# Kernel tuning notes

Hardware: AMD Instinct MI355X
Metric: run time of the kernel (lower is better)

## Reference

```python
import jax, jax.numpy as jnp
import numpy as np

D = 512

def setup_inputs() -> dict:
    key = jax.random.key(0)
    ks = jax.random.split(key, 12)
    B, d, H, W = 128, D, 14, 14
    s = 1.0 / np.sqrt(d)
    s2 = 1.0 / np.sqrt(2 * d)
    return {
        "m_prev": jax.random.normal(ks[0], (B, d), dtype=jnp.float32),
        "KB": jax.random.normal(ks[1], (B, d, H, W), dtype=jnp.float32),
        "c_i": jax.random.normal(ks[2], (B, d), dtype=jnp.float32),
        # Linear params stored as [in, out] so y = x @ W + b
        "W_m": jax.random.uniform(ks[3], (d, d), jnp.float32, -s, s),
        "b_m": jax.random.uniform(ks[4], (d,), jnp.float32, -s, s),
        "W_kb": jax.random.uniform(ks[5], (d, d), jnp.float32, -s, s),
        "b_kb": jax.random.uniform(ks[6], (d,), jnp.float32, -s, s),
        "W_merge": jax.random.uniform(ks[7], (2 * d, d), jnp.float32, -s2, s2),
        "b_merge": jax.random.uniform(ks[8], (d,), jnp.float32, -s2, s2),
        "W_attn": jax.random.uniform(ks[9], (d, 1), jnp.float32, -s, s),
        "b_attn": jax.random.uniform(ks[10], (1,), jnp.float32, -s, s),
    }


def reference(m_prev, KB, c_i, W_m, b_m, W_kb, b_kb, W_merge, b_merge, W_attn, b_attn):
    # m_prev: [B, d], KB: [B, d, H, W], c_i: [B, d]
    B, d, H, W = KB.shape
    KB_hw = jnp.transpose(KB, (0, 2, 3, 1))            # [B, H, W, d]
    _m_prev = (m_prev @ W_m + b_m)[:, None, None, :]   # [B, 1, 1, d]
    _KB = KB_hw @ W_kb + b_kb                          # [B, H, W, d]
    I = _m_prev * _KB                                  # [B, H, W, d]
    # merge: [I; KB] @ W_merge split into two halves to avoid the concat
    _I = I @ W_merge[:d] + KB_hw @ W_merge[d:] + b_merge  # [B, H, W, d]
    I2 = c_i[:, None, None, :] * _I                    # [B, H, W, d]
    mv = I2 @ W_attn + b_attn                          # [B, H, W, 1]
    # weighted spatial sum: sum over H*W of mv * KB_hw -> [B, d]
    m_new = jnp.einsum("bhwo,bhwd->bd", mv, KB_hw)
    return m_new
```

## Files before the change

### kernel.cpp

```cpp
#include <hip/hip_runtime.h>

#define D   512
#define HW  196
#define NS  8
#define MS  16


__global__ void k_stage1(const float* __restrict__ m_prev, const float* __restrict__ W_m,
                         const float* __restrict__ b_m, const float* __restrict__ c,
                         const float* __restrict__ W_attn, const float* __restrict__ W_merge,
                         float* __restrict__ p_part, float* __restrict__ t12_part) {
    const int bx = blockIdx.x;
    const int t  = threadIdx.x;
    __shared__ float xs[16][64];

    if (bx < 128) {
        const int jt = bx & 1, bt = (bx >> 1) & 7, kt = bx >> 4;
        const int j  = jt * 256 + t;
        const int b0 = bt * 16;
        const int k0 = kt * 64;
        for (int i = t; i < 16 * 64; i += 256)
            xs[i >> 6][i & 63] = m_prev[(b0 + (i >> 6)) * D + k0 + (i & 63)];
        __syncthreads();
        float acc[16];
        #pragma unroll
        for (int bb = 0; bb < 16; ++bb) acc[bb] = 0.f;
        for (int kk = 0; kk < 64; ++kk) {
            float wv = W_m[(k0 + kk) * D + j];
            #pragma unroll
            for (int bb = 0; bb < 16; ++bb) acc[bb] += xs[bb][kk] * wv;
        }
        const float bias = (kt == 0) ? b_m[j] : 0.f;
        #pragma unroll
        for (int bb = 0; bb < 16; ++bb)
            p_part[((size_t)kt * 128 + b0 + bb) * D + j] = acc[bb] + bias;
    } else {
        const int i2 = bx - 128;
        const int kkt = i2 & 3, bt = (i2 >> 2) & 7, jt = i2 >> 5;
        const int kk = kkt * 256 + t;
        const int b0 = bt * 16;
        const int j0 = jt * 64;
        for (int i = t; i < 16 * 64; i += 256) {
            int bb = i >> 6, jj = i & 63;
            xs[bb][jj] = c[(b0 + bb) * D + j0 + jj] * W_attn[j0 + jj];
        }
        __syncthreads();
        float acc[16];
        #pragma unroll
        for (int bb = 0; bb < 16; ++bb) acc[bb] = 0.f;
        const float4* wrow = (const float4*)&W_merge[(size_t)kk * D + j0];
        for (int q = 0; q < 16; ++q) {
            float4 w4 = wrow[q];
            #pragma unroll
            for (int bb = 0; bb < 16; ++bb)
                acc[bb] += xs[bb][4*q+0] * w4.x + xs[bb][4*q+1] * w4.y
                         + xs[bb][4*q+2] * w4.z + xs[bb][4*q+3] * w4.w;
        }
        #pragma unroll
        for (int bb = 0; bb < 16; ++bb)
            t12_part[((size_t)jt * 128 + b0 + bb) * 1024 + kk] = acc[bb];
    }
}

__global__ void k_stage2(const float* __restrict__ p_part, const float* __restrict__ t12_part,
                         const float* __restrict__ W_kb, const float* __restrict__ c,
                         const float* __restrict__ W_attn, const float* __restrict__ b_merge,
                         const float* __restrict__ b_kb, const float* __restrict__ b_attn,
                         float* __restrict__ w_part, float* __restrict__ beta) {
    const int bx = blockIdx.x;
    const int t  = threadIdx.x;
    __shared__ float rs[16][64];

    if (bx < 128) {
        const int kpt = bx & 1, bt = (bx >> 1) & 7, kt = bx >> 4;
        const int kp = kpt * 256 + t;
        const int b0 = bt * 16;
        const int k0 = kt * 64;
        for (int i = t; i < 16 * 64; i += 256) {
            int bb = i >> 6, kk = i & 63;
            int b = b0 + bb, k = k0 + kk;
            float pv = 0.f, tv = 0.f;
            #pragma unroll
            for (int s = 0; s < NS; ++s) {
                pv += p_part[((size_t)s * 128 + b) * D + k];
                tv += t12_part[((size_t)s * 128 + b) * 1024 + k];
            }
            rs[bb][kk] = pv * tv;
        }
        __syncthreads();
        float acc[16];
        #pragma unroll
        for (int bb = 0; bb < 16; ++bb) acc[bb] = 0.f;
        const float4* wrow = (const float4*)&W_kb[(size_t)kp * D + k0];
        for (int q = 0; q < 16; ++q) {
            float4 w4 = wrow[q];
            #pragma unroll
            for (int bb = 0; bb < 16; ++bb)
                acc[bb] += rs[bb][4*q+0] * w4.x + rs[bb][4*q+1] * w4.y
                         + rs[bb][4*q+2] * w4.z + rs[bb][4*q+3] * w4.w;
        }
        #pragma unroll
        for (int bb = 0; bb < 16; ++bb) {
            float extra = 0.f;
            if (kt == 0) {
                #pragma unroll
                for (int s = 0; s < NS; ++s)
                    extra += t12_part[((size_t)s * 128 + b0 + bb) * 1024 + 512 + kp];
            }
            w_part[((size_t)kt * 128 + b0 + bb) * D + kp] = acc[bb] + extra;
        }
    } else {
        const int b = bx - 128;
        float sum = 0.f;
        for (int j = t; j < D; j += 256) {
            float pv = 0.f, tv = 0.f;
            #pragma unroll
            for (int s = 0; s < NS; ++s) {
                pv += p_part[((size_t)s * 128 + b) * D + j];
                tv += t12_part[((size_t)s * 128 + b) * 1024 + j];
            }
            float u = c[b * D + j] * W_attn[j];
            sum += b_merge[j] * u + b_kb[j] * (pv * tv);
        }
        #pragma unroll
        for (int off = 32; off; off >>= 1) sum += __shfl_down(sum, off, 64);
        __shared__ float red[4];
        if ((t & 63) == 0) red[t >> 6] = sum;
        __syncthreads();
        if (t == 0) beta[b] = red[0] + red[1] + red[2] + red[3] + b_attn[0];
    }
}

__global__ void k_mv(const float* __restrict__ KB, const float* __restrict__ w_part,
                     float* __restrict__ mvp) {
    const int b  = blockIdx.x >> 4;
    const int ks = blockIdx.x & (MS - 1);
    const int t  = threadIdx.x;
    __shared__ float wl[32];
    if (t < 32) {
        float s = 0.f;
        #pragma unroll
        for (int q = 0; q < NS; ++q)
            s += w_part[((size_t)q * 128 + b) * D + ks * 32 + t];
        wl[t] = s;
    }
    __syncthreads();
    if (t < HW) {
        const float* kbp = KB + (size_t)b * D * HW + (size_t)ks * 32 * HW + t;
        float acc = 0.f;
        #pragma unroll
        for (int k = 0; k < 32; ++k) acc += kbp[(size_t)k * HW] * wl[k];
        mvp[((size_t)b * MS + ks) * HW + t] = acc;
    }
}

__global__ void k_mnew(const float* __restrict__ KB, const float* __restrict__ mvp,
                       const float* __restrict__ beta, float* __restrict__ out) {
    const int b  = blockIdx.x >> 4;
    const int kt = blockIdx.x & 15;
    const int t  = threadIdx.x;
    const int wave = t >> 6, lane = t & 63;
    __shared__ float4 mv4_s[49];

    if (t < HW) {
        float s = beta[b];
        #pragma unroll
        for (int q = 0; q < MS; ++q)
            s += mvp[((size_t)b * MS + q) * HW + t];
        ((float*)mv4_s)[t] = s;
    }
    __syncthreads();

    const float4 m4 = (lane < 49) ? mv4_s[lane] : make_float4(0.f, 0.f, 0.f, 0.f);
    #pragma unroll
    for (int i = 0; i < 8; ++i) {
        const int k = kt * 32 + wave * 8 + i;
        float p = 0.f;
        if (lane < 49) {
            float4 v = ((const float4*)(KB + ((size_t)b * D + k) * HW))[lane];
            p = v.x * m4.x + v.y * m4.y + v.z * m4.z + v.w * m4.w;
        }
        #pragma unroll
        for (int off = 32; off; off >>= 1) p += __shfl_xor(p, off, 64);
        if (lane == 0) out[(size_t)b * D + k] = p;
    }
}

extern "C" void kernel_launch(void* const* d_in, const int* in_sizes, int n_in,
                              void* d_out, int out_size, void* d_ws, size_t ws_size,
                              hipStream_t stream) {
    const float* m_prev  = (const float*)d_in[0];
    const float* KB      = (const float*)d_in[1];
    const float* c_i     = (const float*)d_in[2];
    const float* W_m     = (const float*)d_in[3];
    const float* b_m     = (const float*)d_in[4];
    const float* W_kb    = (const float*)d_in[5];
    const float* b_kb    = (const float*)d_in[6];
    const float* W_merge = (const float*)d_in[7];
    const float* b_merge = (const float*)d_in[8];
    const float* W_attn  = (const float*)d_in[9];
    const float* b_attn  = (const float*)d_in[10];
    float* out = (float*)d_out;

    float* ws       = (float*)d_ws;
    float* p_part   = ws;
    float* t12_part = ws + 524288;
    float* w_part   = ws + 1572864;
    float* beta     = ws + 2097152;
    float* mvp      = ws + 2097280;

    k_stage1<<<384, 256, 0, stream>>>(m_prev, W_m, b_m, c_i, W_attn, W_merge,
                                      p_part, t12_part);
    k_stage2<<<256, 256, 0, stream>>>(p_part, t12_part, W_kb, c_i, W_attn,
                                      b_merge, b_kb, b_attn, w_part, beta);
    k_mv  <<<2048, 256, 0, stream>>>(KB, w_part, mvp);
    k_mnew<<<2048, 256, 0, stream>>>(KB, mvp, beta, out);
}
```

Measured before the change: 51.13 us.

## Fuse stage2 W_kb projection and beta into the KB matvec kernel

```diff
diff --git a/kernel.cpp b/kernel.cpp
--- a/kernel.cpp
+++ b/kernel.cpp
@@ -62,92 +62,69 @@
     }
 }
 
-__global__ void k_stage2(const float* __restrict__ p_part, const float* __restrict__ t12_part,
-                         const float* __restrict__ W_kb, const float* __restrict__ c,
-                         const float* __restrict__ W_attn, const float* __restrict__ b_merge,
-                         const float* __restrict__ b_kb, const float* __restrict__ b_attn,
-                         float* __restrict__ w_part, float* __restrict__ beta) {
-    const int bx = blockIdx.x;
-    const int t  = threadIdx.x;
-    __shared__ float rs[16][64];
+__global__ __launch_bounds__(256, 4)
+void k_wmv(const float* __restrict__ KB, const float* __restrict__ p_part,
+           const float* __restrict__ t12_part, const float* __restrict__ W_kb,
+           const float* __restrict__ c, const float* __restrict__ W_attn,
+           const float* __restrict__ b_merge, const float* __restrict__ b_kb,
+           const float* __restrict__ b_attn, float* __restrict__ mvp) {
+    const int b    = blockIdx.x >> 4;
+    const int ks   = blockIdx.x & (MS - 1);
+    const int t    = threadIdx.x;
+    const int wave = t >> 6, lane = t & 63;
 
-    if (bx < 128) {
-        const int kpt = bx & 1, bt = (bx >> 1) & 7, kt = bx >> 4;
-        const int kp = kpt * 256 + t;
-        const int b0 = bt * 16;
-        const int k0 = kt * 64;
-        for (int i = t; i < 16 * 64; i += 256) {
-            int bb = i >> 6, kk = i & 63;
-            int b = b0 + bb, k = k0 + kk;
-            float pv = 0.f, tv = 0.f;
-            #pragma unroll
-            for (int s = 0; s < NS; ++s) {
-                pv += p_part[((size_t)s * 128 + b) * D + k];
-                tv += t12_part[((size_t)s * 128 + b) * 1024 + k];
-            }
-            rs[bb][kk] = pv * tv;
+    __shared__ float r_s[512];
+    __shared__ float wl[32];
+    __shared__ float winit[32];
+    __shared__ float redB[4];
+
+    for (int k = t; k < 512; k += 256) {
+        float pv = 0.f, tv = 0.f;
+        #pragma unroll
+        for (int s = 0; s < NS; ++s) {
+            pv += p_part[((size_t)s * 128 + b) * D + k];
+            tv += t12_part[((size_t)s * 128 + b) * 1024 + k];
         }
-        __syncthreads();
-        float acc[16];
+        r_s[k] = pv * tv;
+    }
+    if (t < 32) {
+        float s2 = 0.f;
         #pragma unroll
-        for (int bb = 0; bb < 16; ++bb) acc[bb] = 0.f;
-        const float4* wrow = (const float4*)&W_kb[(size_t)kp * D + k0];
-        for (int q = 0; q < 16; ++q) {
-            float4 w4 = wrow[q];
-            #pragma unroll
-            for (int bb = 0; bb < 16; ++bb)
-                acc[bb] += rs[bb][4*q+0] * w4.x + rs[bb][4*q+1] * w4.y
-                         + rs[bb][4*q+2] * w4.z + rs[bb][4*q+3] * w4.w;
-        }
-        #pragma unroll
-        for (int bb = 0; bb < 16; ++bb) {
-            float extra = 0.f;
-            if (kt == 0) {
-                #pragma unroll
-                for (int s = 0; s < NS; ++s)
-                    extra += t12_part[((size_t)s * 128 + b0 + bb) * 1024 + 512 + kp];
-            }
-            w_part[((size_t)kt * 128 + b0 + bb) * D + kp] = acc[bb] + extra;
-        }
-    } else {
-        const int b = bx - 128;
-        float sum = 0.f;
-        for (int j = t; j < D; j += 256) {
-            float pv = 0.f, tv = 0.f;
-            #pragma unroll
-            for (int s = 0; s < NS; ++s) {
-                pv += p_part[((size_t)s * 128 + b) * D + j];
-                tv += t12_part[((size_t)s * 128 + b) * 1024 + j];
-            }
-            float u = c[b * D + j] * W_attn[j];
-            sum += b_merge[j] * u + b_kb[j] * (pv * tv);
-        }
-        #pragma unroll
-        for (int off = 32; off; off >>= 1) sum += __shfl_down(sum, off, 64);
-        __shared__ float red[4];
-        if ((t & 63) == 0) red[t >> 6] = sum;
-        __syncthreads();
-        if (t == 0) beta[b] = red[0] + red[1] + red[2] + red[3] + b_attn[0];
-    }
-}
-
-__global__ void k_mv(const float* __restrict__ KB, const float* __restrict__ w_part,
-                     float* __restrict__ mvp) {
-    const int b  = blockIdx.x >> 4;
-    const int ks = blockIdx.x & (MS - 1);
-    const int t  = threadIdx.x;
-    __shared__ float wl[32];
-    if (t < 32) {
-        float s = 0.f;
-        #pragma unroll
-        for (int q = 0; q < NS; ++q)
-            s += w_part[((size_t)q * 128 + b) * D + ks * 32 + t];
-        wl[t] = s;
+        for (int s = 0; s < NS; ++s)
+            s2 += t12_part[((size_t)s * 128 + b) * 1024 + 512 + ks * 32 + t];
+        winit[t] = s2;
     }
     __syncthreads();
+
+    if (ks == 0) {
+        float bsum = 0.f;
+        for (int k = t; k < 512; k += 256)
+            bsum += b_merge[k] * c[(size_t)b * D + k] * W_attn[k] + b_kb[k] * r_s[k];
+        #pragma unroll
+        for (int off = 32; off; off >>= 1) bsum += __shfl_down(bsum, off, 64);
+        if (lane == 0) redB[wave] = bsum;
+    }
+
+    const float4 ra = *(const float4*)&r_s[lane * 8];
+    const float4 rb = *(const float4*)&r_s[lane * 8 + 4];
+    #pragma unroll
+    for (int i = 0; i < 8; ++i) {
+        const int row = ks * 32 + wave * 8 + i;
+        const float4* wr = (const float4*)&W_kb[(size_t)row * D + lane * 8];
+        float4 w0 = wr[0], w1 = wr[1];
+        float dot = w0.x * ra.x + w0.y * ra.y + w0.z * ra.z + w0.w * ra.w
+                  + w1.x * rb.x + w1.y * rb.y + w1.z * rb.z + w1.w * rb.w;
+        #pragma unroll
+        for (int off = 32; off; off >>= 1) dot += __shfl_down(dot, off, 64);
+        if (lane == 0) wl[wave * 8 + i] = dot + winit[wave * 8 + i];
+    }
+    __syncthreads();
+
+    float beta = 0.f;
+    if (ks == 0) beta = redB[0] + redB[1] + redB[2] + redB[3] + b_attn[0];
     if (t < HW) {
         const float* kbp = KB + (size_t)b * D * HW + (size_t)ks * 32 * HW + t;
-        float acc = 0.f;
+        float acc = beta;
         #pragma unroll
         for (int k = 0; k < 32; ++k) acc += kbp[(size_t)k * HW] * wl[k];
         mvp[((size_t)b * MS + ks) * HW + t] = acc;
@@ -155,7 +132,7 @@
 }
 
 __global__ void k_mnew(const float* __restrict__ KB, const float* __restrict__ mvp,
-                       const float* __restrict__ beta, float* __restrict__ out) {
+                       float* __restrict__ out) {
     const int b  = blockIdx.x >> 4;
     const int kt = blockIdx.x & 15;
     const int t  = threadIdx.x;
@@ -163,7 +140,7 @@
     __shared__ float4 mv4_s[49];
 
     if (t < HW) {
-        float s = beta[b];
+        float s = 0.f;
         #pragma unroll
         for (int q = 0; q < MS; ++q)
             s += mvp[((size_t)b * MS + q) * HW + t];
@@ -205,14 +182,11 @@
     float* ws       = (float*)d_ws;
     float* p_part   = ws;
     float* t12_part = ws + 524288;
-    float* w_part   = ws + 1572864;
-    float* beta     = ws + 2097152;
-    float* mvp      = ws + 2097280;
+    float* mvp      = ws + 1572864;
 
     k_stage1<<<384, 256, 0, stream>>>(m_prev, W_m, b_m, c_i, W_attn, W_merge,
                                       p_part, t12_part);
-    k_stage2<<<256, 256, 0, stream>>>(p_part, t12_part, W_kb, c_i, W_attn,
-                                      b_merge, b_kb, b_attn, w_part, beta);
-    k_mv  <<<2048, 256, 0, stream>>>(KB, w_part, mvp);
-    k_mnew<<<2048, 256, 0, stream>>>(KB, mvp, beta, out);
+    k_wmv  <<<2048, 256, 0, stream>>>(KB, p_part, t12_part, W_kb, c_i, W_attn,
+                                      b_merge, b_kb, b_attn, mvp);
+    k_mnew <<<2048, 256, 0, stream>>>(KB, mvp, out);
 }
```

Result: faster. 46.06 us (-9.9%).
